# Performance work log

Hardware: AMD Instinct MI355X
Metric: run time of the kernel (lower is better)

The kernel has to match this reference:

```python
import jax, jax.numpy as jnp
import numpy as np

INHIBITION_INCREASE = 5.0
DECAY_RATE = 100.0
DECAY_SIGMA = 5.0
DT = 0.001
DT_SQRT = float(np.sqrt(DT))


def setup_inputs() -> dict:
    key = jax.random.key(0)
    k1, k2 = jax.random.split(key)
    inputs = jax.random.normal(k1, (8192, 2048), dtype=jnp.float32)
    inhibition = jax.random.normal(k2, (8192, 1), dtype=jnp.float32)
    return {"inputs": inputs, "inhibition": inhibition}


def reference(inputs, inhibition):
    key = jax.random.key(42)
    kn, ku, kc = jax.random.split(key, 3)
    # inhibition decay + diffusion noise (Euler-Maruyama step)
    inhib = (1.0 - DECAY_RATE * DT) * inhibition + DECAY_SIGMA * DT_SQRT * jax.random.normal(kn, inhibition.shape, dtype=inhibition.dtype)
    # instantaneous firing rates, clipped for numerical safety
    rates = jnp.clip(jnp.exp(inputs - inhib), 1e-20, 1e20)  # [B, N]
    total_rate = jnp.sum(rates, axis=-1, keepdims=True)      # [B, 1]
    rand_val = jax.random.uniform(ku, total_rate.shape, dtype=total_rate.dtype)
    spike_occurred = rand_val < DT * total_rate               # [B, 1] bool
    # categorical over rates == categorical with logits log(rates)
    spike_location = jax.random.categorical(kc, jnp.log(rates), axis=-1)  # [B]
    out_spike_locations = jax.nn.one_hot(spike_location, rates.shape[-1], dtype=inputs.dtype)  # [B, N]
    out_spikes = out_spike_locations * spike_occurred.astype(inputs.dtype)  # [B, N]
    inhib = inhib + jnp.max(out_spikes, axis=-1, keepdims=True) * INHIBITION_INCREASE
    return out_spikes, inhib
```

## Files before the change

kernel.cpp:

```cpp
#include <hip/hip_runtime.h>
#include <cstdint>
#include <cmath>

#define N_ROWS 8192
#define N_COLS 2048
#define OUT_SPIKES_ELEMS (N_ROWS * N_COLS)

__host__ __device__ inline uint32_t rotl32(uint32_t x, int d) {
#if defined(__HIP_DEVICE_COMPILE__)
  return __builtin_amdgcn_alignbit(x, x, 32u - (uint32_t)d);
#else
  return (x << d) | (x >> (32 - d));
#endif
}

__host__ __device__ inline void threefry2x32(uint32_t k0, uint32_t k1,
                                             uint32_t x0, uint32_t x1,
                                             uint32_t& o0, uint32_t& o1) {
  const uint32_t ks2 = k0 ^ k1 ^ 0x1BD11BDAu;
  x0 += k0; x1 += k1;
#define TFR(r) { x0 += x1; x1 = rotl32(x1, (r)); x1 ^= x0; }
  TFR(13) TFR(15) TFR(26) TFR(6)
  x0 += k1; x1 += ks2 + 1u;
  TFR(17) TFR(29) TFR(16) TFR(24)
  x0 += ks2; x1 += k0 + 2u;
  TFR(13) TFR(15) TFR(26) TFR(6)
  x0 += k0; x1 += k1 + 3u;
  TFR(17) TFR(29) TFR(16) TFR(24)
  x0 += k1; x1 += ks2 + 4u;
  TFR(13) TFR(15) TFR(26) TFR(6)
  x0 += ks2; x1 += k0 + 5u;
#undef TFR
  o0 = x0; o1 = x1;
}

__device__ inline uint32_t random_bits32(uint32_t k0, uint32_t k1, uint32_t j) {
  uint32_t o0, o1;
  threefry2x32(k0, k1, 0u, j, o0, o1);
  return o0 ^ o1;
}

__device__ inline float unit_from_bits(uint32_t bits) {
  return __uint_as_float((bits >> 9) | 0x3f800000u) - 1.0f;
}

__device__ inline float xla_erfinv(float x) {
  float w = -log1pf(__fmul_rn(-x, x));
  float p;
  if (w < 5.0f) {
    w = __fadd_rn(w, -2.5f);
    p = 2.81022636e-08f;
    p = __fadd_rn(3.43273939e-07f,  __fmul_rn(p, w));
    p = __fadd_rn(-3.5233877e-06f,  __fmul_rn(p, w));
    p = __fadd_rn(-4.39150654e-06f, __fmul_rn(p, w));
    p = __fadd_rn(0.00021858087f,   __fmul_rn(p, w));
    p = __fadd_rn(-0.00125372503f,  __fmul_rn(p, w));
    p = __fadd_rn(-0.00417768164f,  __fmul_rn(p, w));
    p = __fadd_rn(0.246640727f,     __fmul_rn(p, w));
    p = __fadd_rn(1.50140941f,      __fmul_rn(p, w));
  } else {
    w = __fadd_rn(sqrtf(w), -3.0f);
    p = -0.000200214257f;
    p = __fadd_rn(0.000100950558f,  __fmul_rn(p, w));
    p = __fadd_rn(0.00134934322f,   __fmul_rn(p, w));
    p = __fadd_rn(-0.00367342844f,  __fmul_rn(p, w));
    p = __fadd_rn(0.00573950773f,   __fmul_rn(p, w));
    p = __fadd_rn(-0.0076224613f,   __fmul_rn(p, w));
    p = __fadd_rn(0.00943887047f,   __fmul_rn(p, w));
    p = __fadd_rn(1.00167406f,      __fmul_rn(p, w));
    p = __fadd_rn(2.83297682f,      __fmul_rn(p, w));
  }
  return __fmul_rn(p, x);
}

__device__ inline float normal_from_bits(uint32_t bits) {
  const float lo = -0.99999994f;
  float unit = unit_from_bits(bits);
  float t = __fadd_rn(__fmul_rn(unit, 2.0f), lo);
  t = fmaxf(lo, t);
  return __fmul_rn(1.4142135623730951f, xla_erfinv(t));
}

__global__ __launch_bounds__(256) void row_setup_kernel(
    const float* __restrict__ inhibition, float* __restrict__ ws, float csig,
    uint32_t kn0, uint32_t kn1, uint32_t ku0, uint32_t ku1) {
  int r = blockIdx.x * 256 + threadIdx.x;
  if (r >= N_ROWS) return;
  float nrm = normal_from_bits(random_bits32(kn0, kn1, (uint32_t)r));
  float ih = __fadd_rn(__fmul_rn(0.9f, inhibition[r]), __fmul_rn(csig, nrm));
  float pre = expf(-ih);
  float ur  = unit_from_bits(random_bits32(ku0, ku1, (uint32_t)r));
  reinterpret_cast<float4*>(ws)[r] = make_float4(ih, pre, ur, 0.0f);
}

__global__ __launch_bounds__(256, 6) void spike_kernel(
    const float* __restrict__ inputs, const float* __restrict__ ws,
    float* __restrict__ out, uint32_t kc0, uint32_t kc1) {
  const int row = blockIdx.x;
  const int tid = threadIdx.x;
  const int wid = tid >> 6;
  const float tiny = 1.17549435e-38f;
  const float nln2 = -0.69314718055994531f;
  const float log2e = 1.4426950408889634f;

  __shared__ uint2 stash[8 * 256];
  __shared__ float s_sum[4];
  __shared__ float s_cv[4];
  __shared__ int   s_ci[4];
  __shared__ int   s_final[2];

  const float* rowp = inputs + (size_t)row * N_COLS;
  const float4* rowp4 = reinterpret_cast<const float4*>(rowp);
  float4 a0 = rowp4[tid];
  float4 a1 = rowp4[tid + 256];
  float xv[8] = {a0.x, a0.y, a0.z, a0.w, a1.x, a1.y, a1.z, a1.w};

  float vmaxA = -INFINITY, vmaxB = -INFINITY;
  float tsA = 0.0f, tsB = 0.0f;
  const uint32_t jbase = (uint32_t)(row * N_COLS + 4 * tid);

#pragma unroll
  for (int i8 = 0; i8 < 8; ++i8) {
    const uint32_t j = jbase + (uint32_t)((i8 & 3) + 1024 * (i8 >> 2));
    uint32_t bits = random_bits32(kc0, kc1, j);
    float u = unit_from_bits(bits);
    float t = __fadd_rn(u, tiny);
    float m = __log2f(t);
    float v = fmaf(nln2, __log2f(-m), xv[i8]);
    stash[i8 * 256 + tid] = make_uint2(bits, __float_as_uint(v));
    float e = __builtin_amdgcn_exp2f(__fmul_rn(xv[i8], log2e));
    if (i8 & 1) { vmaxB = fmaxf(vmaxB, v); tsB += e; }
    else        { vmaxA = fmaxf(vmaxA, v); tsA += e; }
  }
  const float tmax = fmaxf(vmaxA, vmaxB);
  float vmax = tmax;
  float tsum = tsA + tsB;

#pragma unroll
  for (int off = 32; off > 0; off >>= 1) {
    tsum += __shfl_xor(tsum, off);
    vmax = fmaxf(vmax, __shfl_xor(vmax, off));
  }
  const float thrM = __fsub_rn(vmax, 1e-3f);

  float cval = -INFINITY;
  int   cidx = 0x7fffffff;
  if (tmax >= thrM) {
    float ih = ws[4 * row];
#pragma unroll
    for (int i8 = 0; i8 < 8; ++i8) {
      uint2 s = stash[i8 * 256 + tid];
      if (__uint_as_float(s.y) >= thrM) {
        int col = 4 * tid + 1024 * (i8 >> 2) + (i8 & 3);
        float t = __fadd_rn(unit_from_bits(s.x), tiny);
        float g = -logf(-logf(t));
        float x = __fsub_rn(rowp[col], ih);
        float v = __fadd_rn(g, x);
        if (v > cval || (v == cval && col < cidx)) { cval = v; cidx = col; }
      }
    }
  }

#pragma unroll
  for (int off = 32; off > 0; off >>= 1) {
    float ov = __shfl_xor(cval, off);
    int   oi = __shfl_xor(cidx, off);
    if (ov > cval || (ov == cval && oi < cidx)) { cval = ov; cidx = oi; }
  }

  if ((tid & 63) == 0) { s_sum[wid] = tsum; s_cv[wid] = cval; s_ci[wid] = cidx; }
  __syncthreads();

  if (tid == 0) {
    float T = s_sum[0] + s_sum[1] + s_sum[2] + s_sum[3];
    float bv = s_cv[0];
    int   bi = s_ci[0];
    for (int w = 1; w < 4; ++w) {
      if (s_cv[w] > bv || (s_cv[w] == bv && s_ci[w] < bi)) { bv = s_cv[w]; bi = s_ci[w]; }
    }
    float4 wsd = reinterpret_cast<const float4*>(ws)[row];
    double total = (double)T * (double)wsd.y;
    float thr = __fmul_rn(0.001f, (float)total);
    int spike = (wsd.z < thr) ? 1 : 0;
    s_final[0] = bi;
    s_final[1] = spike;
    out[OUT_SPIKES_ELEMS + row] = spike ? __fadd_rn(wsd.x, 5.0f) : wsd.x;
  }
  __syncthreads();

  const int bi = s_final[0];
  const int spike = s_final[1];
  float* orow = out + (size_t)row * N_COLS;
#pragma unroll
  for (int ch = 0; ch < 2; ++ch) {
    const int col = 4 * tid + 1024 * ch;
    float4 z = make_float4(0.f, 0.f, 0.f, 0.f);
    if (spike && bi >= col && bi < col + 4) {
      (&z.x)[bi - col] = 1.0f;
    }
    *reinterpret_cast<float4*>(orow + col) = z;
  }
}

extern "C" void kernel_launch(void* const* d_in, const int* in_sizes, int n_in,
                              void* d_out, int out_size, void* d_ws, size_t ws_size,
                              hipStream_t stream) {
  const float* inputs     = (const float*)d_in[0];
  const float* inhibition = (const float*)d_in[1];
  float* out = (float*)d_out;
  float* ws  = (float*)d_ws;

  uint32_t kn0, kn1, ku0, ku1, kc0, kc1;
  threefry2x32(0u, 42u, 0u, 0u, kn0, kn1);
  threefry2x32(0u, 42u, 0u, 1u, ku0, ku1);
  threefry2x32(0u, 42u, 0u, 2u, kc0, kc1);

  const float csig = (float)(5.0 * sqrt(0.001));

  hipLaunchKernelGGL(row_setup_kernel, dim3(N_ROWS / 256), dim3(256), 0, stream,
                     inhibition, ws, csig, kn0, kn1, ku0, ku1);
  hipLaunchKernelGGL(spike_kernel, dim3(N_ROWS), dim3(256), 0, stream,
                     inputs, ws, out, kc0, kc1);
}
```

Measured before the change: 57.25 us.

## Use DPP wave reductions and shared 64-bit atomicMax for argmax selection

```diff
diff --git a/kernel.cpp b/kernel.cpp
--- a/kernel.cpp
+++ b/kernel.cpp
@@ -81,6 +81,32 @@
   return __fmul_rn(1.4142135623730951f, xla_erfinv(t));
 }
 
+__device__ __forceinline__ float wave_sum_bcast(float x) {
+  x += __int_as_float(__builtin_amdgcn_update_dpp(0, __float_as_int(x), 0x111, 0xf, 0xf, true));
+  x += __int_as_float(__builtin_amdgcn_update_dpp(0, __float_as_int(x), 0x112, 0xf, 0xf, true));
+  x += __int_as_float(__builtin_amdgcn_update_dpp(0, __float_as_int(x), 0x114, 0xf, 0xf, true));
+  x += __int_as_float(__builtin_amdgcn_update_dpp(0, __float_as_int(x), 0x118, 0xf, 0xf, true));
+  x += __int_as_float(__builtin_amdgcn_update_dpp(0, __float_as_int(x), 0x142, 0xa, 0xf, true));
+  x += __int_as_float(__builtin_amdgcn_update_dpp(0, __float_as_int(x), 0x143, 0xc, 0xf, true));
+  return __int_as_float(__builtin_amdgcn_readlane(__float_as_int(x), 63));
+}
+__device__ __forceinline__ float wave_max_bcast(float x) {
+  int xi;
+  xi = __float_as_int(x);
+  x = fmaxf(x, __int_as_float(__builtin_amdgcn_update_dpp(xi, xi, 0x111, 0xf, 0xf, false)));
+  xi = __float_as_int(x);
+  x = fmaxf(x, __int_as_float(__builtin_amdgcn_update_dpp(xi, xi, 0x112, 0xf, 0xf, false)));
+  xi = __float_as_int(x);
+  x = fmaxf(x, __int_as_float(__builtin_amdgcn_update_dpp(xi, xi, 0x114, 0xf, 0xf, false)));
+  xi = __float_as_int(x);
+  x = fmaxf(x, __int_as_float(__builtin_amdgcn_update_dpp(xi, xi, 0x118, 0xf, 0xf, false)));
+  xi = __float_as_int(x);
+  x = fmaxf(x, __int_as_float(__builtin_amdgcn_update_dpp(xi, xi, 0x142, 0xa, 0xf, false)));
+  xi = __float_as_int(x);
+  x = fmaxf(x, __int_as_float(__builtin_amdgcn_update_dpp(xi, xi, 0x143, 0xc, 0xf, false)));
+  return __int_as_float(__builtin_amdgcn_readlane(__float_as_int(x), 63));
+}
+
 __global__ __launch_bounds__(256) void row_setup_kernel(
     const float* __restrict__ inhibition, float* __restrict__ ws, float csig,
     uint32_t kn0, uint32_t kn1, uint32_t ku0, uint32_t ku1) {
@@ -105,9 +131,9 @@
 
   __shared__ uint2 stash[8 * 256];
   __shared__ float s_sum[4];
-  __shared__ float s_cv[4];
-  __shared__ int   s_ci[4];
-  __shared__ int   s_final[2];
+  __shared__ unsigned long long s_best;
+
+  if (tid == 0) s_best = 0ull;
 
   const float* rowp = inputs + (size_t)row * N_COLS;
   const float4* rowp4 = reinterpret_cast<const float4*>(rowp);
@@ -133,18 +159,14 @@
     else        { vmaxA = fmaxf(vmaxA, v); tsA += e; }
   }
   const float tmax = fmaxf(vmaxA, vmaxB);
-  float vmax = tmax;
-  float tsum = tsA + tsB;
-
-#pragma unroll
-  for (int off = 32; off > 0; off >>= 1) {
-    tsum += __shfl_xor(tsum, off);
-    vmax = fmaxf(vmax, __shfl_xor(vmax, off));
-  }
+
+  float tsum = wave_sum_bcast(tsA + tsB);
+  float vmax = wave_max_bcast(tmax);
+  if ((tid & 63) == 0) s_sum[wid] = tsum;
   const float thrM = __fsub_rn(vmax, 1e-3f);
 
-  float cval = -INFINITY;
-  int   cidx = 0x7fffffff;
+  __syncthreads();
+
   if (tmax >= thrM) {
     float ih = ws[4 * row];
 #pragma unroll
@@ -156,40 +178,25 @@
         float g = -logf(-logf(t));
         float x = __fsub_rn(rowp[col], ih);
         float v = __fadd_rn(g, x);
-        if (v > cval || (v == cval && col < cidx)) { cval = v; cidx = col; }
+        uint32_t b = __float_as_uint(v);
+        uint32_t key = (b & 0x80000000u) ? ~b : (b | 0x80000000u);
+        unsigned long long pk =
+            ((unsigned long long)key << 32) | (uint32_t)(~(uint32_t)col);
+        atomicMax(&s_best, pk);
       }
     }
   }
 
-#pragma unroll
-  for (int off = 32; off > 0; off >>= 1) {
-    float ov = __shfl_xor(cval, off);
-    int   oi = __shfl_xor(cidx, off);
-    if (ov > cval || (ov == cval && oi < cidx)) { cval = ov; cidx = oi; }
-  }
-
-  if ((tid & 63) == 0) { s_sum[wid] = tsum; s_cv[wid] = cval; s_ci[wid] = cidx; }
   __syncthreads();
 
-  if (tid == 0) {
-    float T = s_sum[0] + s_sum[1] + s_sum[2] + s_sum[3];
-    float bv = s_cv[0];
-    int   bi = s_ci[0];
-    for (int w = 1; w < 4; ++w) {
-      if (s_cv[w] > bv || (s_cv[w] == bv && s_ci[w] < bi)) { bv = s_cv[w]; bi = s_ci[w]; }
-    }
-    float4 wsd = reinterpret_cast<const float4*>(ws)[row];
-    double total = (double)T * (double)wsd.y;
-    float thr = __fmul_rn(0.001f, (float)total);
-    int spike = (wsd.z < thr) ? 1 : 0;
-    s_final[0] = bi;
-    s_final[1] = spike;
-    out[OUT_SPIKES_ELEMS + row] = spike ? __fadd_rn(wsd.x, 5.0f) : wsd.x;
-  }
-  __syncthreads();
-
-  const int bi = s_final[0];
-  const int spike = s_final[1];
+  const int bi = (int)(~(uint32_t)(s_best & 0xFFFFFFFFull));
+  float T = ((s_sum[0] + s_sum[1]) + s_sum[2]) + s_sum[3];
+  float4 wsd = reinterpret_cast<const float4*>(ws)[row];
+  double total = (double)T * (double)wsd.y;
+  float thr = __fmul_rn(0.001f, (float)total);
+  const int spike = (wsd.z < thr) ? 1 : 0;
+  if (tid == 0) out[OUT_SPIKES_ELEMS + row] = spike ? __fadd_rn(wsd.x, 5.0f) : wsd.x;
+
   float* orow = out + (size_t)row * N_COLS;
 #pragma unroll
   for (int ch = 0; ch < 2; ++ch) {
```

Result: faster. 49.79 us, median of 2 (-13.0%).
